# Optimization experiments

Measured on AMD Instinct MI355X. Metric: run time of the kernel, lower is better.

Reference implementation:

```python
import jax, jax.numpy as jnp
import numpy as np
from jax import lax

B, C, XH, XW, KH, KW = 32, 128, 96, 96, 3, 3
BN_EPS = 1e-5


def setup_inputs() -> dict:
    key = jax.random.key(0)
    k1, k2, k3 = jax.random.split(key, 3)
    x = jax.random.normal(k1, (B, C, XH, XW), dtype=jnp.float32)
    k = jax.random.normal(k2, (B, C, KH, KW), dtype=jnp.float32)
    pw_weight = jax.random.normal(k3, (C, C), dtype=jnp.float32) * (1.0 / np.sqrt(C))
    bn_gamma = jnp.ones((C,), dtype=jnp.float32)
    bn_beta = jnp.zeros((C,), dtype=jnp.float32)
    bn_mean = jnp.zeros((C,), dtype=jnp.float32)
    bn_var = jnp.ones((C,), dtype=jnp.float32)
    return {"x": x, "k": k, "pw_weight": pw_weight, "bn_gamma": bn_gamma,
            "bn_beta": bn_beta, "bn_mean": bn_mean, "bn_var": bn_var}


def _depthwise_one(xi, ki):
    # xi: [C, XH, XW], ki: [C, KH, KW] -> per-sample depthwise conv, padding=KH//2
    pad = KH // 2
    out = lax.conv_general_dilated(
        xi[None],                 # [1, C, XH, XW]
        ki[:, None],              # [C, 1, KH, KW]  (OIHW with groups=C)
        window_strides=(1, 1),
        padding=((pad, pad), (pad, pad)),
        feature_group_count=C,
        dimension_numbers=("NCHW", "OIHW", "NCHW"),
    )
    return out[0]


def reference(x, k, pw_weight, bn_gamma, bn_beta, bn_mean, bn_var):
    # Per-sample dynamic depthwise conv, batched via vmap (replaces the Python loop)
    x_new = jax.vmap(_depthwise_one)(x, k)          # [B, C, XH, XW]
    # 1x1 pointwise conv (no bias)
    y = jnp.einsum("bchw,oc->bohw", x_new, pw_weight)
    # BatchNorm (inference form with running stats) + ReLU
    inv = bn_gamma * lax.rsqrt(bn_var + BN_EPS)
    y = y * inv[None, :, None, None] + (bn_beta - bn_mean * inv)[None, :, None, None]
    return jax.nn.relu(y)
```

## Files before the change

kernel.cpp:

```cpp
#include <hip/hip_runtime.h>
#include <hip/hip_bf16.h>

#define BB 32
#define CC 128
#define HH 96
#define WW 96
#define BN_EPS 1e-5f

typedef __attribute__((ext_vector_type(8))) short bf16x8_t;
typedef __attribute__((ext_vector_type(4))) float f32x4_t;
typedef __attribute__((ext_vector_type(4), aligned(4))) float f32x4u_t;
typedef __attribute__((ext_vector_type(2))) unsigned int u32x2_t;
typedef __attribute__((ext_vector_type(4))) unsigned int u32x4_t;

__global__ __launch_bounds__(256)
void prep_kernel(const float* __restrict__ pw,
                 const float* __restrict__ g, const float* __restrict__ b,
                 const float* __restrict__ m, const float* __restrict__ v,
                 unsigned short* __restrict__ wper,
                 float* __restrict__ inv, float* __restrict__ bias)
{
    int t = blockIdx.x * 256 + threadIdx.x;
    if (t < CC * CC) {
        int o = t >> 7, cidx = t & 127;
        int kc = cidx >> 5, r = cidx & 31, gg = r >> 3, j = r & 7;
        int c = kc * 32 + gg * 4 + (j & 3) + 16 * (j >> 2);
        __hip_bfloat16 h = __float2bfloat16(pw[o * CC + c]);
        wper[o * CC + cidx] = *reinterpret_cast<unsigned short*>(&h);
    }
    if (t < CC) {
        float iv = g[t] * rsqrtf(v[t] + BN_EPS);
        inv[t] = iv;
        bias[t] = b[t] - m[t] * iv;
    }
}

__global__ __launch_bounds__(256, 6)
void dw_kernel(const float* __restrict__ x, const float* __restrict__ kk,
               unsigned short* __restrict__ xn)
{
    const int u = blockIdx.x * 256 + threadIdx.x;
    const int lane = threadIdx.x & 63;
    const int woct = u % 12;
    int t1 = u / 12;
    const int cs = t1 & 127;
    int t2 = t1 >> 7;
    const int th = t2 % 12;
    const int b  = t2 / 12;

    const int kc = cs >> 5, rr = cs & 31, gg = rr >> 3, jj = rr & 7;
    const int c = kc * 32 + gg * 4 + (jj & 3) + 16 * (jj >> 2);

    const int w0 = woct * 8;
    const int h0 = th * 8;
    const bool l_edge = (woct == 0);
    const bool r_edge = (woct == 11);

    const float* plane = x + (size_t)(b * CC + c) * (HH * WW);

    float kw[9];
    {
        const float* kp = kk + (size_t)(b * CC + c) * 9;
        f32x4u_t q0 = *(const f32x4u_t*)(kp);
        f32x4u_t q1 = *(const f32x4u_t*)(kp + 4);
        kw[0]=q0.x; kw[1]=q0.y; kw[2]=q0.z; kw[3]=q0.w;
        kw[4]=q1.x; kw[5]=q1.y; kw[6]=q1.z; kw[7]=q1.w;
        kw[8]=kp[8];
    }

    float rA[10], rB[10], rC[10];
    auto load_row = [&](int row, float* o) {
        const bool valid = (row >= 0) && (row < HH);
        const int rrow = row < 0 ? 0 : (row >= HH ? HH - 1 : row);
        const float* rp = plane + rrow * WW + w0;
        f32x4_t M0 = *(const f32x4_t*)rp;
        f32x4_t M1 = *(const f32x4_t*)(rp + 4);
        float vl = __shfl_up(M1.w, 1);
        float vr = __shfl_down(M0.x, 1);
        if (lane == 0  && !l_edge) vl = rp[-1];
        if (lane == 63 && !r_edge) vr = rp[8];
        o[0] = (valid && !l_edge) ? vl : 0.f;
        o[1] = valid ? M0.x : 0.f;
        o[2] = valid ? M0.y : 0.f;
        o[3] = valid ? M0.z : 0.f;
        o[4] = valid ? M0.w : 0.f;
        o[5] = valid ? M1.x : 0.f;
        o[6] = valid ? M1.y : 0.f;
        o[7] = valid ? M1.z : 0.f;
        o[8] = valid ? M1.w : 0.f;
        o[9] = (valid && !r_edge) ? vr : 0.f;
    };

    load_row(h0 - 1, rA);
    load_row(h0,     rB);

    unsigned short* dst0 = xn + ((size_t)(b * CC + cs) * (HH * WW) + (size_t)h0 * WW + w0);

    #pragma unroll
    for (int py = 0; py < 8; ++py) {
        load_row(h0 + py + 1, rC);

        unsigned pkw[4];
        #pragma unroll
        for (int i = 0; i < 4; ++i) {
            float s0 = 0.f, s1 = 0.f;
            #pragma unroll
            for (int t = 0; t < 3; ++t) {
                s0 = fmaf(rA[2 * i + t],     kw[t],     s0);
                s0 = fmaf(rB[2 * i + t],     kw[3 + t], s0);
                s0 = fmaf(rC[2 * i + t],     kw[6 + t], s0);
                s1 = fmaf(rA[2 * i + 1 + t], kw[t],     s1);
                s1 = fmaf(rB[2 * i + 1 + t], kw[3 + t], s1);
                s1 = fmaf(rC[2 * i + 1 + t], kw[6 + t], s1);
            }
            __hip_bfloat16 h0b = __float2bfloat16(s0);
            __hip_bfloat16 h1b = __float2bfloat16(s1);
            pkw[i] = (unsigned)*reinterpret_cast<unsigned short*>(&h0b)
                   | ((unsigned)*reinterpret_cast<unsigned short*>(&h1b) << 16);
        }
        u32x4_t pk;
        pk.x = pkw[0]; pk.y = pkw[1]; pk.z = pkw[2]; pk.w = pkw[3];
        *reinterpret_cast<u32x4_t*>(dst0 + (size_t)py * WW) = pk;

        #pragma unroll
        for (int t = 0; t < 10; ++t) { rA[t] = rB[t]; rB[t] = rC[t]; }
    }
}

__global__ __launch_bounds__(256, 3)
void pw_kernel(const unsigned short* __restrict__ xn,
               const unsigned short* __restrict__ wper,
               const float* __restrict__ invp, const float* __restrict__ biasp,
               float* __restrict__ out)
{
    __shared__ __align__(16) unsigned char xnb[128 * 256];
    const int tid = threadIdx.x;

    const unsigned wg  = blockIdx.x;
    const unsigned nid = (wg & 7u) * 96u + (wg >> 3);
    const int tw  = nid % 6u;
    const int thg = (nid / 6u) % 4u;
    const int b   = nid / 24u;
    const int w0  = tw * 16;

    const int lane   = tid & 63;
    const int wv     = tid >> 6;
    const int lo     = lane & 15;
    const int hi     = lane >> 4;
    const int o_base = wv * 32;

    bf16x8_t wfrag[2][4];
    #pragma unroll
    for (int t2 = 0; t2 < 2; ++t2)
        #pragma unroll
        for (int kc = 0; kc < 4; ++kc)
            wfrag[t2][kc] = *reinterpret_cast<const bf16x8_t*>(
                wper + (size_t)(o_base + t2 * 16 + lo) * CC + kc * 32 + hi * 8);

    float iv2[2], bs2[2];
    #pragma unroll
    for (int t2 = 0; t2 < 2; ++t2) {
        iv2[t2] = invp[o_base + t2 * 16 + lo];
        bs2[t2] = biasp[o_base + t2 * 16 + lo];
    }

    const int cs4 = tid >> 3;
    const int py  = tid & 7;
    const unsigned short* src_base =
        xn + (size_t)(b * CC + cs4 * 4) * (HH * WW) + (size_t)py * WW + w0;

    unsigned dLA[4][4], dRA[4][4], dLB[4][4], dRB[4][4];

    auto LOADREGS = [&](int t, unsigned (*dL)[4], unsigned (*dR)[4]) {
        const unsigned short* s0 = src_base + (size_t)((thg * 3 + t) * 8) * WW;
        #pragma unroll
        for (int q = 0; q < 4; ++q) {
            const unsigned short* src = s0 + (size_t)q * (HH * WW);
            u32x4_t L = *(const u32x4_t*)src;
            u32x4_t R = *(const u32x4_t*)(src + 8);
            dL[q][0]=L.x; dL[q][1]=L.y; dL[q][2]=L.z; dL[q][3]=L.w;
            dR[q][0]=R.x; dR[q][1]=R.y; dR[q][2]=R.z; dR[q][3]=R.w;
        }
    };

    auto WRITE_LDS = [&](unsigned (*dL)[4], unsigned (*dR)[4]) {
        #pragma unroll
        for (int o8 = 0; o8 < 2; ++o8) {
            #pragma unroll
            for (int j = 0; j < 4; ++j) {
                const unsigned d0 = o8 ? dR[0][j] : dL[0][j];
                const unsigned d1 = o8 ? dR[1][j] : dL[1][j];
                const unsigned d2 = o8 ? dR[2][j] : dL[2][j];
                const unsigned d3 = o8 ? dR[3][j] : dL[3][j];
                u32x2_t we, wo;
                we.x = __builtin_amdgcn_perm(d1, d0, 0x05040100u);
                we.y = __builtin_amdgcn_perm(d3, d2, 0x05040100u);
                wo.x = __builtin_amdgcn_perm(d1, d0, 0x07060302u);
                wo.y = __builtin_amdgcn_perm(d3, d2, 0x07060302u);
                const int pe = py * 16 + o8 * 8 + 2 * j;
                const int po = pe + 1;
                *reinterpret_cast<u32x2_t*>(&xnb[(unsigned)pe * 256 +
                    (((unsigned)cs4 * 8) ^ (((unsigned)pe & 7u) << 4))]) = we;
                *reinterpret_cast<u32x2_t*>(&xnb[(unsigned)po * 256 +
                    (((unsigned)cs4 * 8) ^ (((unsigned)po & 7u) << 4))]) = wo;
            }
        }
    };

    auto COMPUTE = [&](int t) {
        const int h0 = (thg * 3 + t) * 8;
        f32x4_t acc[8][2];
        #pragma unroll
        for (int pt = 0; pt < 8; ++pt) {
            acc[pt][0] = (f32x4_t){0.f, 0.f, 0.f, 0.f};
            acc[pt][1] = (f32x4_t){0.f, 0.f, 0.f, 0.f};
        }
        #pragma unroll
        for (int pt = 0; pt < 8; ++pt) {
            const unsigned rowbase = (unsigned)(pt * 16 + lo) * 256;
            const unsigned sw = (unsigned)((lo & 7) << 4);
            #pragma unroll
            for (int kc = 0; kc < 4; ++kc) {
                bf16x8_t xfrag = *reinterpret_cast<const bf16x8_t*>(
                    &xnb[rowbase + (((unsigned)(kc * 64 + hi * 16)) ^ sw)]);
                acc[pt][0] = __builtin_amdgcn_mfma_f32_16x16x32_bf16(
                    xfrag, wfrag[0][kc], acc[pt][0], 0, 0, 0);
                acc[pt][1] = __builtin_amdgcn_mfma_f32_16x16x32_bf16(
                    xfrag, wfrag[1][kc], acc[pt][1], 0, 0, 0);
            }
        }
        #pragma unroll
        for (int pt = 0; pt < 8; ++pt) {
            const int hrow = h0 + pt;
            #pragma unroll
            for (int t2 = 0; t2 < 2; ++t2) {
                const int o = o_base + t2 * 16 + lo;
                f32x4_t vv;
                #pragma unroll
                for (int r = 0; r < 4; ++r)
                    vv[r] = fmaxf(fmaf(acc[pt][t2][r], iv2[t2], bs2[t2]), 0.f);
                __builtin_nontemporal_store(vv, reinterpret_cast<f32x4_t*>(
                    out + ((size_t)(b * CC + o) * HH + hrow) * WW + w0 + hi * 4));
            }
        }
    };

    LOADREGS(0, dLA, dRA);
    WRITE_LDS(dLA, dRA);
    LOADREGS(1, dLB, dRB);
    __syncthreads();
    COMPUTE(0);
    __syncthreads();
    WRITE_LDS(dLB, dRB);
    LOADREGS(2, dLA, dRA);
    __syncthreads();
    COMPUTE(1);
    __syncthreads();
    WRITE_LDS(dLA, dRA);
    __syncthreads();
    COMPUTE(2);
}

__global__ __launch_bounds__(256, 3)
void fused_main(const float* __restrict__ x, const float* __restrict__ kk,
                const unsigned short* __restrict__ wper,
                const float* __restrict__ invp, const float* __restrict__ biasp,
                float* __restrict__ out)
{
    __shared__ __align__(16) unsigned char xnb[128 * 256];
    const int tid = threadIdx.x;
    const unsigned wg  = blockIdx.x;
    const unsigned nid = (wg & 7u) * 288u + (wg >> 3);
    const int bx = nid % 6u;
    const int by = (nid / 6u) % 12u;
    const int bb = nid / 72u;
    const int w0 = bx * 16;
    const int h0 = by * 8;
    {
        const int wq = tid & 3;
        const int cp = tid >> 2;
        const int s  = cp << 1;
        const int kc = s >> 5, rr = s & 31, gg = rr >> 3, jj = rr & 7;
        const int cA = kc * 32 + gg * 4 + (jj & 3) + 16 * (jj >> 2);
        const int gw = w0 + wq * 4;
        const bool l_edge = (gw == 0);
        const bool r_edge = (gw + 4 >= WW);
        const float* planeA = x + (size_t)(bb * CC + cA) * (HH * WW);
        float kwA[9], kwB[9];
        {
            const float* kp = kk + (size_t)(bb * CC + cA) * 9;
            f32x4u_t q0 = *(const f32x4u_t*)(kp + 0);
            f32x4u_t q1 = *(const f32x4u_t*)(kp + 4);
            f32x4u_t q2 = *(const f32x4u_t*)(kp + 8);
            f32x4u_t q3 = *(const f32x4u_t*)(kp + 12);
            float     e16 = kp[16], e17 = kp[17];
            kwA[0]=q0.x; kwA[1]=q0.y; kwA[2]=q0.z; kwA[3]=q0.w;
            kwA[4]=q1.x; kwA[5]=q1.y; kwA[6]=q1.z; kwA[7]=q1.w;
            kwA[8]=q2.x;
            kwB[0]=q2.y; kwB[1]=q2.z; kwB[2]=q2.w;
            kwB[3]=q3.x; kwB[4]=q3.y; kwB[5]=q3.z; kwB[6]=q3.w;
            kwB[7]=e16;  kwB[8]=e17;
        }
        float xd[2][10][6];
        #pragma unroll
        for (int q = 0; q < 2; ++q) {
            const float* plane = planeA + q * (HH * WW);
            #pragma unroll
            for (int r = 0; r < 10; ++r) {
                const int row = h0 - 1 + r;
                const bool valid = (row >= 0) && (row < HH);
                const int rrow = row < 0 ? 0 : (row >= HH ? HH - 1 : row);
                const float* rp = plane + rrow * WW + gw;
                f32x4_t M = *(const f32x4_t*)rp;
                float vl = rp[l_edge ? 0 : -1];
                float vr = rp[r_edge ? 3 : 4];
                xd[q][r][0] = (valid && !l_edge) ? vl : 0.f;
                xd[q][r][1] = valid ? M.x : 0.f;
                xd[q][r][2] = valid ? M.y : 0.f;
                xd[q][r][3] = valid ? M.z : 0.f;
                xd[q][r][4] = valid ? M.w : 0.f;
                xd[q][r][5] = (valid && !r_edge) ? vr : 0.f;
            }
        }
        #pragma unroll
        for (int py = 0; py < 8; ++py) {
            #pragma unroll
            for (int i = 0; i < 4; ++i) {
                float sA = 0.f, sB = 0.f;
                #pragma unroll
                for (int t = 0; t < 3; ++t) {
                    sA = fmaf(xd[0][py + 0][i + t], kwA[t],     sA);
                    sA = fmaf(xd[0][py + 1][i + t], kwA[3 + t], sA);
                    sA = fmaf(xd[0][py + 2][i + t], kwA[6 + t], sA);
                    sB = fmaf(xd[1][py + 0][i + t], kwB[t],     sB);
                    sB = fmaf(xd[1][py + 1][i + t], kwB[3 + t], sB);
                    sB = fmaf(xd[1][py + 2][i + t], kwB[6 + t], sB);
                }
                __hip_bfloat16 hA = __float2bfloat16(sA);
                __hip_bfloat16 hB = __float2bfloat16(sB);
                unsigned pk = (unsigned)*reinterpret_cast<unsigned short*>(&hA)
                            | ((unsigned)*reinterpret_cast<unsigned short*>(&hB) << 16);
                const int p = py * 16 + wq * 4 + i;
                const unsigned boff = ((unsigned)(cp << 2)) ^ (((unsigned)p & 7u) << 4);
                *reinterpret_cast<unsigned*>(&xnb[(unsigned)p * 256 + boff]) = pk;
            }
        }
    }
    __syncthreads();
    {
        const int lane   = tid & 63;
        const int wv     = tid >> 6;
        const int lo     = lane & 15;
        const int hi     = lane >> 4;
        const int o_base = wv * 32;
        bf16x8_t afrag[2][4];
        #pragma unroll
        for (int t2 = 0; t2 < 2; ++t2)
            #pragma unroll
            for (int kc = 0; kc < 4; ++kc)
                afrag[t2][kc] = *reinterpret_cast<const bf16x8_t*>(
                    wper + (size_t)(o_base + t2 * 16 + lo) * CC + kc * 32 + hi * 8);
        f32x4_t acc[8][2];
        #pragma unroll
        for (int pt = 0; pt < 8; ++pt) {
            acc[pt][0] = (f32x4_t){0.f, 0.f, 0.f, 0.f};
            acc[pt][1] = (f32x4_t){0.f, 0.f, 0.f, 0.f};
        }
        #pragma unroll
        for (int pt = 0; pt < 8; ++pt) {
            const unsigned rowbase = (unsigned)(pt * 16 + lo) * 256;
            const unsigned sw = (unsigned)((lo & 7) << 4);
            #pragma unroll
            for (int kc = 0; kc < 4; ++kc) {
                bf16x8_t bfrag = *reinterpret_cast<const bf16x8_t*>(
                    &xnb[rowbase + (((unsigned)(kc * 64 + hi * 16)) ^ sw)]);
                acc[pt][0] = __builtin_amdgcn_mfma_f32_16x16x32_bf16(
                    afrag[0][kc], bfrag, acc[pt][0], 0, 0, 0);
                acc[pt][1] = __builtin_amdgcn_mfma_f32_16x16x32_bf16(
                    afrag[1][kc], bfrag, acc[pt][1], 0, 0, 0);
            }
        }
        float iv[2][4], bs[2][4];
        #pragma unroll
        for (int t2 = 0; t2 < 2; ++t2)
            #pragma unroll
            for (int r = 0; r < 4; ++r) {
                const int o = o_base + t2 * 16 + hi * 4 + r;
                iv[t2][r] = invp[o];
                bs[t2][r] = biasp[o];
            }
        #pragma unroll
        for (int pt = 0; pt < 8; ++pt) {
            const int hrow = h0 + pt;
            #pragma unroll
            for (int t2 = 0; t2 < 2; ++t2) {
                #pragma unroll
                for (int r = 0; r < 4; ++r) {
                    const int o = o_base + t2 * 16 + hi * 4 + r;
                    float val = fmaf(acc[pt][t2][r], iv[t2][r], bs[t2][r]);
                    val = fmaxf(val, 0.f);
                    out[((size_t)(bb * CC + o) * HH + hrow) * WW + w0 + lo] = val;
                }
            }
        }
    }
}

extern "C" void kernel_launch(void* const* d_in, const int* in_sizes, int n_in,
                              void* d_out, int out_size, void* d_ws, size_t ws_size,
                              hipStream_t stream) {
    const float* x   = (const float*)d_in[0];
    const float* kk  = (const float*)d_in[1];
    const float* pwt = (const float*)d_in[2];
    const float* g   = (const float*)d_in[3];
    const float* b   = (const float*)d_in[4];
    const float* m   = (const float*)d_in[5];
    const float* v   = (const float*)d_in[6];
    float* out = (float*)d_out;

    unsigned short* wper = (unsigned short*)d_ws;
    float* inv  = (float*)((char*)d_ws + 32768);
    float* bias = (float*)((char*)d_ws + 32768 + 512);
    unsigned short* xn = (unsigned short*)((char*)d_ws + 36864);
    const size_t need = 36864 + (size_t)BB * CC * HH * WW * 2;

    prep_kernel<<<64, 256, 0, stream>>>(pwt, g, b, m, v, wper, inv, bias);
    if (ws_size >= need) {
        dw_kernel<<<dim3(2304), 256, 0, stream>>>(x, kk, xn);
        pw_kernel<<<dim3(768), 256, 0, stream>>>(xn, wper, inv, bias, out);
    } else {
        fused_main<<<dim3(2304), 256, 0, stream>>>(x, kk, wper, inv, bias, out);
    }
}
```

Baseline: 104.1 us.

## Compute one output row per thread in depthwise kernel with XCD-aware block remap

```diff
diff --git a/kernel.cpp b/kernel.cpp
--- a/kernel.cpp
+++ b/kernel.cpp
@@ -39,20 +39,21 @@
 void dw_kernel(const float* __restrict__ x, const float* __restrict__ kk,
                unsigned short* __restrict__ xn)
 {
-    const int u = blockIdx.x * 256 + threadIdx.x;
+    const unsigned wg  = blockIdx.x;
+    const unsigned bid = (wg & 7u) * 2304u + (wg >> 3);
+    const int u = (int)bid * 256 + threadIdx.x;
     const int lane = threadIdx.x & 63;
     const int woct = u % 12;
     int t1 = u / 12;
-    const int cs = t1 & 127;
-    int t2 = t1 >> 7;
-    const int th = t2 % 12;
-    const int b  = t2 / 12;
+    const int h = t1 % HH;
+    int t2 = t1 / HH;
+    const int cs = t2 & 127;
+    const int b  = t2 >> 7;
 
     const int kc = cs >> 5, rr = cs & 31, gg = rr >> 3, jj = rr & 7;
     const int c = kc * 32 + gg * 4 + (jj & 3) + 16 * (jj >> 2);
 
     const int w0 = woct * 8;
-    const int h0 = th * 8;
     const bool l_edge = (woct == 0);
     const bool r_edge = (woct == 11);
 
@@ -68,7 +69,7 @@
         kw[8]=kp[8];
     }
 
-    float rA[10], rB[10], rC[10];
+    float r0[10], r1[10], r2[10];
     auto load_row = [&](int row, float* o) {
         const bool valid = (row >= 0) && (row < HH);
         const int rrow = row < 0 ? 0 : (row >= HH ? HH - 1 : row);
@@ -91,40 +92,32 @@
         o[9] = (valid && !r_edge) ? vr : 0.f;
     };
 
-    load_row(h0 - 1, rA);
-    load_row(h0,     rB);
-
-    unsigned short* dst0 = xn + ((size_t)(b * CC + cs) * (HH * WW) + (size_t)h0 * WW + w0);
-
+    load_row(h - 1, r0);
+    load_row(h,     r1);
+    load_row(h + 1, r2);
+
+    unsigned pkw[4];
     #pragma unroll
-    for (int py = 0; py < 8; ++py) {
-        load_row(h0 + py + 1, rC);
-
-        unsigned pkw[4];
-        #pragma unroll
-        for (int i = 0; i < 4; ++i) {
-            float s0 = 0.f, s1 = 0.f;
-            #pragma unroll
-            for (int t = 0; t < 3; ++t) {
-                s0 = fmaf(rA[2 * i + t],     kw[t],     s0);
-                s0 = fmaf(rB[2 * i + t],     kw[3 + t], s0);
-                s0 = fmaf(rC[2 * i + t],     kw[6 + t], s0);
-                s1 = fmaf(rA[2 * i + 1 + t], kw[t],     s1);
-                s1 = fmaf(rB[2 * i + 1 + t], kw[3 + t], s1);
-                s1 = fmaf(rC[2 * i + 1 + t], kw[6 + t], s1);
-            }
-            __hip_bfloat16 h0b = __float2bfloat16(s0);
-            __hip_bfloat16 h1b = __float2bfloat16(s1);
-            pkw[i] = (unsigned)*reinterpret_cast<unsigned short*>(&h0b)
-                   | ((unsigned)*reinterpret_cast<unsigned short*>(&h1b) << 16);
-        }
-        u32x4_t pk;
-        pk.x = pkw[0]; pk.y = pkw[1]; pk.z = pkw[2]; pk.w = pkw[3];
-        *reinterpret_cast<u32x4_t*>(dst0 + (size_t)py * WW) = pk;
-
-        #pragma unroll
-        for (int t = 0; t < 10; ++t) { rA[t] = rB[t]; rB[t] = rC[t]; }
-    }
+    for (int i = 0; i < 4; ++i) {
+        float s0 = 0.f, s1 = 0.f;
+        #pragma unroll
+        for (int t = 0; t < 3; ++t) {
+            s0 = fmaf(r0[2 * i + t],     kw[t],     s0);
+            s0 = fmaf(r1[2 * i + t],     kw[3 + t], s0);
+            s0 = fmaf(r2[2 * i + t],     kw[6 + t], s0);
+            s1 = fmaf(r0[2 * i + 1 + t], kw[t],     s1);
+            s1 = fmaf(r1[2 * i + 1 + t], kw[3 + t], s1);
+            s1 = fmaf(r2[2 * i + 1 + t], kw[6 + t], s1);
+        }
+        __hip_bfloat16 h0b = __float2bfloat16(s0);
+        __hip_bfloat16 h1b = __float2bfloat16(s1);
+        pkw[i] = (unsigned)*reinterpret_cast<unsigned short*>(&h0b)
+               | ((unsigned)*reinterpret_cast<unsigned short*>(&h1b) << 16);
+    }
+    u32x4_t pk;
+    pk.x = pkw[0]; pk.y = pkw[1]; pk.z = pkw[2]; pk.w = pkw[3];
+    unsigned short* dst = xn + ((size_t)(b * CC + cs) * (HH * WW) + (size_t)h * WW + w0);
+    *reinterpret_cast<u32x4_t*>(dst) = pk;
 }
 
 __global__ __launch_bounds__(256, 3)
@@ -426,7 +419,7 @@
 
     prep_kernel<<<64, 256, 0, stream>>>(pwt, g, b, m, v, wper, inv, bias);
     if (ws_size >= need) {
-        dw_kernel<<<dim3(2304), 256, 0, stream>>>(x, kk, xn);
+        dw_kernel<<<dim3(18432), 256, 0, stream>>>(x, kk, xn);
         pw_kernel<<<dim3(768), 256, 0, stream>>>(xn, wper, inv, bias, out);
     } else {
         fused_main<<<dim3(2304), 256, 0, stream>>>(x, kk, wper, inv, bias, out);
```

After: 98.84 us. 5.1% less time.
